# Kernel tuning notes

Measured on AMD Instinct MI355X. Metric: run time of the kernel, lower is better.

The kernel has to match this reference:

```python
import jax, jax.numpy as jnp
import numpy as np

BOX_WARP = 1.0
RAY_START = 2.25
RAY_END = 3.3
S = 32  # depth_resolution (coarse), N_importance = 0


def bilinear_sample(image, coords):
    """Faithful port of the custom grid_sample (align_corners=True mapping).
    image: [B, C, H, W]; coords: [B, M, 2] in [-1, 1]. Returns [B, M, C]."""
    B, C, H, W = image.shape
    ix = (coords[..., 0] + 1.0) * 0.5 * (W - 1)
    iy = (coords[..., 1] + 1.0) * 0.5 * (H - 1)
    ix0 = jnp.floor(ix)
    iy0 = jnp.floor(iy)
    ix1 = ix0 + 1.0
    iy1 = iy0 + 1.0
    # weights use UNclamped corner positions, matching the torch code
    w_nw = (ix1 - ix) * (iy1 - iy)
    w_ne = (ix - ix0) * (iy1 - iy)
    w_sw = (ix1 - ix) * (iy - iy0)
    w_se = (ix - ix0) * (iy - iy0)
    ix0c = jnp.clip(ix0, 0, W - 1).astype(jnp.int32)
    ix1c = jnp.clip(ix1, 0, W - 1).astype(jnp.int32)
    iy0c = jnp.clip(iy0, 0, H - 1).astype(jnp.int32)
    iy1c = jnp.clip(iy1, 0, H - 1).astype(jnp.int32)
    img = image.reshape(B, C, H * W)

    def gather(iyc, ixc):
        idx = iyc * W + ixc  # [B, M]
        return jnp.take_along_axis(img, idx[:, None, :], axis=2)  # [B, C, M]

    out = (gather(iy0c, ix0c) * w_nw[:, None, :]
           + gather(iy0c, ix1c) * w_ne[:, None, :]
           + gather(iy1c, ix0c) * w_sw[:, None, :]
           + gather(iy1c, ix1c) * w_se[:, None, :])
    return out.transpose(0, 2, 1)  # [B, M, C]


def setup_inputs() -> dict:
    key = jax.random.key(0)
    k1, k2, k3, k4, k5 = jax.random.split(key, 5)
    N, n_planes, C, H, W = 2, 3, 32, 256, 256
    R = 16384
    vol_planes = jax.random.normal(k1, (N, n_planes, C, H, W), dtype=jnp.float32)
    dirs = jax.random.normal(k2, (N, R, 3), dtype=jnp.float32)
    dirs = dirs / jnp.linalg.norm(dirs, axis=-1, keepdims=True)
    # camera on sphere of radius 2.7 looking through origin -> samples in box
    ray_origins = -2.7 * dirs
    w1 = jax.random.normal(k3, (C, 64), dtype=jnp.float32) * (1.0 / np.sqrt(C))
    b1 = jnp.zeros((64,), dtype=jnp.float32)
    w2 = jax.random.normal(k4, (64, 33), dtype=jnp.float32) * (1.0 / 8.0)
    b2 = jnp.zeros((33,), dtype=jnp.float32)
    return {"vol_planes": vol_planes, "ray_origins": ray_origins,
            "ray_directions": dirs, "w1": w1, "b1": b1, "w2": w2, "b2": b2}


def reference(vol_planes, ray_origins, ray_directions, w1, b1, w2, b2):
    N, n_planes, C, H, W = vol_planes.shape
    R = ray_origins.shape[1]
    # --- sample_stratified (deterministic: midpoint of each bin) ---
    t = (jnp.arange(S, dtype=vol_planes.dtype) + 0.5) / S
    d = RAY_START + (RAY_END - RAY_START) * t  # [S]
    depths = jnp.broadcast_to(d[None, None, :, None], (N, R, S, 1))
    coords = ray_origins[:, :, None, :] + depths * ray_directions[:, :, None, :]
    M = R * S
    coords = coords.reshape(N, M, 3) * (2.0 / BOX_WARP)
    # --- project_onto_planes (vol_proj=True): xyz, yzx, xzy; sampler uses xy ---
    xy = coords[..., jnp.array([0, 1])]
    yz = coords[..., jnp.array([1, 2])]
    xz = coords[..., jnp.array([0, 2])]
    proj = jnp.stack([xy, yz, xz], axis=1).reshape(N * n_planes, M, 2)
    feats = bilinear_sample(vol_planes.reshape(N * n_planes, C, H, W), proj)
    feats = feats.reshape(N, n_planes, M, C).mean(axis=1)  # aggregate planes
    # --- decoder: small MLP -> 1 sigma + 32 rgb features (EG3D style) ---
    h = jax.nn.softplus(feats @ w1 + b1)
    o = h @ w2 + b2
    sigma = o[..., :1].reshape(N, R, S, 1)
    rgb = (jax.nn.sigmoid(o[..., 1:]) * 1.002 - 0.001).reshape(N, R, S, 32)
    # --- MipRayMarcher2 ---
    deltas = depths[:, :, 1:] - depths[:, :, :-1]
    colors_mid = 0.5 * (rgb[:, :, :-1] + rgb[:, :, 1:])
    densities_mid = 0.5 * (sigma[:, :, :-1] + sigma[:, :, 1:])
    densities_mid = jax.nn.softplus(densities_mid - 1.0)
    alpha = 1.0 - jnp.exp(-deltas * densities_mid)  # [N,R,S-1,1]
    trans = jnp.cumprod(
        jnp.concatenate([jnp.ones_like(alpha[:, :, :1]), 1.0 - alpha + 1e-10],
                        axis=2), axis=2)[:, :, :-1]
    weights = alpha * trans
    rgb_final = (weights * colors_mid).sum(axis=2)  # [N, R, 32]
    return rgb_final
```

## Files before the change

### kernel.cpp

```cpp
#include <hip/hip_runtime.h>
#include <math.h>

#define HH 256
#define WW 256
#define CC 32
#define SS 32
#define NRAYS 32768
#define RPB 8
#define TEXOFF 256

#define FXB_OFF 0
#define SIG_OFF 20480
#define WST_OFF 21504
#define W2T_OFF 25600
#define ALP_OFF 31744
#define POOLSZ  32768

typedef __attribute__((ext_vector_type(8))) short short8;
typedef __attribute__((ext_vector_type(4))) float f32x4;

__device__ __forceinline__ f32x4 mfma16(short8 a, short8 b, f32x4 c) {
    return __builtin_amdgcn_mfma_f32_16x16x32_bf16(a, b, c, 0, 0, 0);
}

__device__ __forceinline__ float bf2f(unsigned short u) {
    union { unsigned int ui; float f; } v; v.ui = ((unsigned int)u) << 16; return v.f;
}
__device__ __forceinline__ float lo2f(unsigned int w) {
    union { unsigned int ui; float f; } v; v.ui = w << 16; return v.f;
}
__device__ __forceinline__ float hi2f(unsigned int w) {
    union { unsigned int ui; float f; } v; v.ui = w & 0xffff0000u; return v.f;
}
__device__ __forceinline__ unsigned short f2bf(float f) {
    union { float f; unsigned int u; } v; v.f = f;
    unsigned int u = v.u;
    unsigned int r = u + 0x7fffu + ((u >> 16) & 1u);
    return (unsigned short)(r >> 16);
}
__device__ __forceinline__ unsigned int pk_bf16(float a, float b) {
    return (unsigned int)f2bf(a) | ((unsigned int)f2bf(b) << 16);
}
__device__ __forceinline__ int iclamp(int x, int lo, int hi) {
    return x < lo ? lo : (x > hi ? hi : x);
}
__device__ __forceinline__ float softplus_f(float z) {
    return fmaxf(z, 0.f) + log1pf(expf(-fabsf(z)));
}
__device__ __forceinline__ float softplus_fast(float z) {
    return fmaxf(z, 0.f) + __logf(1.0f + __expf(-fabsf(z)));
}
__device__ __forceinline__ float sigmoid_fast(float z) {
    return __builtin_amdgcn_rcpf(1.0f + __expf(-z));
}

template<bool F32>
__device__ __forceinline__ float ldv(const void* p, size_t i) {
    if (F32) return ((const float*)p)[i];
    else     return bf2f(((const unsigned short*)p)[i]);
}

__global__ void detect_dtype(const void* __restrict__ rayo, int* __restrict__ flag) {
    const int t = threadIdx.x;
    float sf = 0.f, sb = 0.f;
    if (t < 8) {
        const float* f = (const float*)rayo;
        const unsigned short* u = (const unsigned short*)rayo;
        const float a = f[3 * t], b = f[3 * t + 1], c = f[3 * t + 2];
        const float nf = a * a + b * b + c * c;
        sf = fminf(fabsf(nf - 7.29f), 1e3f);
        const float x = bf2f(u[3 * t]), y = bf2f(u[3 * t + 1]), z = bf2f(u[3 * t + 2]);
        const float nb = x * x + y * y + z * z;
        sb = fminf(fabsf(nb - 7.29f), 1e3f);
    }
    sf += __shfl_down(sf, 4); sb += __shfl_down(sb, 4);
    sf += __shfl_down(sf, 2); sb += __shfl_down(sb, 2);
    sf += __shfl_down(sf, 1); sb += __shfl_down(sb, 1);
    if (t == 0 && blockIdx.x == 0) *flag = (sf < sb) ? 1 : 0;
}

__global__ __launch_bounds__(1024) void transpose_tex(
    const void* __restrict__ vol, unsigned short* __restrict__ tex,
    const int* __restrict__ flag) {
    __shared__ __align__(16) unsigned short tb[32][129];
    const int l = threadIdx.x;
    const int tx = l & 31, ty = l >> 5;
    const int wq = l >> 3, cq = l & 7;
    const int w0 = blockIdx.x * 128;
    const int h  = blockIdx.y;
    const int img = blockIdx.z;
    const size_t srcE = (((size_t)img * CC + ty) * HH + h) * WW + w0 + 4 * tx;
    const size_t dstE = (((size_t)img * HH + h) * WW + (w0 + wq)) * CC + 4 * cq;
    if (*flag) {
        const float4 v = *(const float4*)((const float*)vol + srcE);
        tb[ty][4 * tx + 0] = f2bf(v.x); tb[ty][4 * tx + 1] = f2bf(v.y);
        tb[ty][4 * tx + 2] = f2bf(v.z); tb[ty][4 * tx + 3] = f2bf(v.w);
    } else {
        *(ushort4*)&tb[ty][4 * tx] = *(const ushort4*)((const unsigned short*)vol + srcE);
    }
    __syncthreads();
    ushort4 o;
    o.x = tb[4 * cq + 0][wq]; o.y = tb[4 * cq + 1][wq];
    o.z = tb[4 * cq + 2][wq]; o.w = tb[4 * cq + 3][wq];
    *(ushort4*)(tex + dstE) = o;
}

template<bool F32>
__device__ void render_mfma_body(
    const unsigned short* __restrict__ tex,
    const void* __restrict__ rayo, const void* __restrict__ rayd,
    const void* __restrict__ w1b, const void* __restrict__ b1b,
    const void* __restrict__ w2b, const void* __restrict__ b2b,
    void* __restrict__ outp, char* __restrict__ pool)
{
    const int t = threadIdx.x;
    unsigned short* fxB = (unsigned short*)(pool + FXB_OFF);
    float* sigL = (float*)(pool + SIG_OFF);
    unsigned short* w1t = (unsigned short*)(pool + WST_OFF);
    unsigned short* w2t = (unsigned short*)(pool + W2T_OFF);
    float* aL = (float*)(pool + ALP_OFF);

    for (int i = t; i < 2048; i += 256) {
        const int n = i >> 5, k = i & 31;
        w1t[i] = f2bf(ldv<F32>(w1b, (size_t)k * 64 + n));
    }
    for (int i = t; i < 3072; i += 256) {
        const int n = i >> 6, k = i & 63;
        w2t[i] = (n < 33) ? f2bf(ldv<F32>(w2b, (size_t)k * 33 + n)) : (unsigned short)0;
    }
    __syncthreads();

    {
        const int rl = t >> 5;
        const int L  = t & 31;
        const int c4 = L & 7;
        const int sub = L >> 3;
        const int gray = blockIdx.x * RPB + rl;
        const int n = gray >> 14;
        const size_t rb = (size_t)gray * 3;
        const float ox = ldv<F32>(rayo, rb), oy = ldv<F32>(rayo, rb + 1), oz = ldv<F32>(rayo, rb + 2);
        const float dx = ldv<F32>(rayd, rb), dy = ldv<F32>(rayd, rb + 1), dz = ldv<F32>(rayd, rb + 2);
        const char* texb = (const char*)tex;
        const unsigned int cb = (unsigned int)c4 * 8;

        #pragma unroll 2
        for (int k = 0; k < 8; ++k) {
            const int s = sub * 8 + k;
            const float d = 2.25f + 1.05f * ((s + 0.5f) * (1.0f / 32.0f));
            const float x = (ox + d * dx) * 2.0f;
            const float y = (oy + d * dy) * 2.0f;
            const float z = (oz + d * dz) * 2.0f;
            float a0[4] = {0.f, 0.f, 0.f, 0.f};
            float a1[4] = {0.f, 0.f, 0.f, 0.f};
            float a2[4] = {0.f, 0.f, 0.f, 0.f};
            #pragma unroll
            for (int p = 0; p < 3; p++) {
                const float u = (p == 0) ? x : ((p == 1) ? y : x);
                const float v = (p == 0) ? y : z;
                const float ixf = fmaf(u, 127.5f, 127.5f);
                const float iyf = fmaf(v, 127.5f, 127.5f);
                const float ix0f = floorf(ixf), iy0f = floorf(iyf);
                const float wx1 = ixf - ix0f, wy1 = iyf - iy0f;
                const float wx0 = 1.f - wx1,  wy0 = 1.f - wy1;
                const int ix0 = iclamp((int)ix0f, 0, 255);
                const int ix1 = iclamp((int)ix0f + 1, 0, 255);
                const int iy0 = iclamp((int)iy0f, 0, 255);
                const int iy1 = iclamp((int)iy0f + 1, 0, 255);
                const float w00 = wx0 * wy0, w01 = wx1 * wy0, w10 = wx0 * wy1, w11 = wx1 * wy1;
                const unsigned int pb = (unsigned int)(n * 3 + p) * (HH * WW * CC * 2) + cb;
                const uint2 q00 = *(const uint2*)(texb + pb + ((unsigned int)(iy0 * WW + ix0) << 6));
                const uint2 q01 = *(const uint2*)(texb + pb + ((unsigned int)(iy0 * WW + ix1) << 6));
                const uint2 q10 = *(const uint2*)(texb + pb + ((unsigned int)(iy1 * WW + ix0) << 6));
                const uint2 q11 = *(const uint2*)(texb + pb + ((unsigned int)(iy1 * WW + ix1) << 6));
                const float v00[4] = { lo2f(q00.x), hi2f(q00.x), lo2f(q00.y), hi2f(q00.y) };
                const float v01[4] = { lo2f(q01.x), hi2f(q01.x), lo2f(q01.y), hi2f(q01.y) };
                const float v10[4] = { lo2f(q10.x), hi2f(q10.x), lo2f(q10.y), hi2f(q10.y) };
                const float v11[4] = { lo2f(q11.x), hi2f(q11.x), lo2f(q11.y), hi2f(q11.y) };
                #pragma unroll
                for (int i = 0; i < 4; i++) {
                    float acc = w00 * v00[i];
                    acc = fmaf(w01, v01[i], acc);
                    acc = fmaf(w10, v10[i], acc);
                    acc = fmaf(w11, v11[i], acc);
                    if (p == 0) a0[i] = acc; else if (p == 1) a1[i] = acc; else a2[i] = acc;
                }
            }
            uint2 pk;
            pk.x = pk_bf16((a0[0] + a1[0] + a2[0]) * (1.0f / 3.0f),
                           (a0[1] + a1[1] + a2[1]) * (1.0f / 3.0f));
            pk.y = pk_bf16((a0[2] + a1[2] + a2[2]) * (1.0f / 3.0f),
                           (a0[3] + a1[3] + a2[3]) * (1.0f / 3.0f));
            *(uint2*)(pool + FXB_OFF + (rl * 32 + s) * 80 + c4 * 8) = pk;
        }
    }

    const int w = t >> 6;
    const int lane = t & 63;
    const int l16 = lane & 15, quad = lane >> 4;

    short8 b1f[4];
    #pragma unroll
    for (int nt = 0; nt < 4; nt++)
        b1f[nt] = *(const short8*)(pool + WST_OFF + (nt * 16 + l16) * 64 + quad * 16);
    short8 b2f[3][2];
    #pragma unroll
    for (int nt = 0; nt < 3; nt++)
        #pragma unroll
        for (int ks = 0; ks < 2; ks++)
            b2f[nt][ks] = *(const short8*)(pool + W2T_OFF + (nt * 16 + l16) * 128 + ks * 64 + quad * 16);
    float bb1[4], bb2[3];
    #pragma unroll
    for (int nt = 0; nt < 4; nt++) bb1[nt] = ldv<F32>(b1b, nt * 16 + l16);
    #pragma unroll
    for (int nt = 0; nt < 3; nt++) {
        const int n2 = nt * 16 + l16;
        bb2[nt] = (n2 < 33) ? ldv<F32>(b2b, n2) : 0.f;
    }
    __syncthreads();

    {
        char* hb = pool + WST_OFF + w * 2304;
        #pragma unroll 1
        for (int mt = 0; mt < 4; mt++) {
            const int rbase = w * 64 + mt * 16;
            const short8 a1 = *(const short8*)(pool + FXB_OFF + (rbase + l16) * 80 + quad * 16);
            #pragma unroll
            for (int nt = 0; nt < 4; nt++) {
                f32x4 hc = { bb1[nt], bb1[nt], bb1[nt], bb1[nt] };
                hc = mfma16(a1, b1f[nt], hc);
                #pragma unroll
                for (int r = 0; r < 4; r++) {
                    const float hv = softplus_fast(hc[r]);
                    *(unsigned short*)(hb + (quad * 4 + r) * 144 + (nt * 16 + l16) * 2) = f2bf(hv);
                }
            }
            const short8 a2k0 = *(const short8*)(hb + l16 * 144 + quad * 16);
            const short8 a2k1 = *(const short8*)(hb + l16 * 144 + 64 + quad * 16);
            #pragma unroll
            for (int nt = 0; nt < 3; nt++) {
                f32x4 o = { bb2[nt], bb2[nt], bb2[nt], bb2[nt] };
                o = mfma16(a2k0, b2f[nt][0], o);
                o = mfma16(a2k1, b2f[nt][1], o);
                #pragma unroll
                for (int r = 0; r < 4; r++) {
                    const int row = rbase + quad * 4 + r;
                    if (nt == 0) {
                        if (l16 == 0) sigL[row] = o[r];
                        else fxB[row * 40 + (l16 - 1)] =
                                 f2bf(fmaf(sigmoid_fast(o[r]), 1.002f, -0.001f));
                    } else if (nt == 1) {
                        fxB[row * 40 + (15 + l16)] =
                                 f2bf(fmaf(sigmoid_fast(o[r]), 1.002f, -0.001f));
                    } else if (l16 == 0) {
                        fxB[row * 40 + 31] =
                                 f2bf(fmaf(sigmoid_fast(o[r]), 1.002f, -0.001f));
                    }
                }
            }
        }
    }
    __syncthreads();

    {
        const int rl = t >> 5, sm = t & 31;
        if (sm < 31) {
            const float sp = sigL[rl * 32 + sm];
            const float sn = sigL[rl * 32 + sm + 1];
            const float m = 0.5f * (sp + sn) - 1.0f;
            const float dens = fmaxf(m, 0.f) + __logf(1.0f + __expf(-fabsf(m)));
            aL[rl * 32 + sm] = 1.0f - __expf(-(1.05f / 32.0f) * dens);
        }
    }
    __syncthreads();

    {
        const int rl = t >> 5, sm = t & 31;
        if (sm == 0) {
            float T = 1.0f;
            #pragma unroll
            for (int j = 0; j < 31; j++) {
                const float a = aL[rl * 32 + j];
                aL[rl * 32 + j] = (a * T) * 0.5f;
                T *= (1.0f - a + 1e-10f);
            }
        }
    }
    __syncthreads();

    {
        const int rl = t >> 5, c = t & 31;
        const int gr2 = blockIdx.x * RPB + rl;
        float acc = 0.0f;
        float rp = bf2f(fxB[(rl * 32 + 0) * 40 + c]);
        #pragma unroll 4
        for (int sm = 0; sm < 31; sm++) {
            const float rn = bf2f(fxB[(rl * 32 + sm + 1) * 40 + c]);
            acc = fmaf(aL[rl * 32 + sm], rp + rn, acc);
            rp = rn;
        }
        const size_t oidx = (size_t)gr2 * 32 + c;
        if (F32) ((float*)outp)[oidx] = acc;
        else     ((unsigned short*)outp)[oidx] = f2bf(acc);
    }
}

__global__ __launch_bounds__(256, 4) void render_fast(
    const unsigned short* __restrict__ tex, const void* __restrict__ rayo,
    const void* __restrict__ rayd, const void* __restrict__ w1b,
    const void* __restrict__ b1b, const void* __restrict__ w2b,
    const void* __restrict__ b2b, void* __restrict__ outp,
    const int* __restrict__ flag)
{
    __shared__ __align__(16) char pool[POOLSZ];
    if (*flag) render_mfma_body<true >(tex, rayo, rayd, w1b, b1b, w2b, b2b, outp, pool);
    else       render_mfma_body<false>(tex, rayo, rayd, w1b, b1b, w2b, b2b, outp, pool);
}

template<bool F32>
__device__ __forceinline__ void render_body(
    const void* __restrict__ vol, const void* __restrict__ rayo,
    const void* __restrict__ rayd, const void* __restrict__ w1b,
    const void* __restrict__ b1b, const void* __restrict__ w2b,
    const void* __restrict__ b2b, void* __restrict__ outp,
    float* wsm, float (*rgbL)[SS][33], float (*sigL)[SS])
{
    const int t = threadIdx.x;
    for (int i = t; i < 4257; i += 256) {
        float v;
        if (i < 2048)       v = ldv<F32>(w1b, i);
        else if (i < 2112)  v = ldv<F32>(b1b, i - 2048);
        else if (i < 4224)  v = ldv<F32>(w2b, i - 2112);
        else                v = ldv<F32>(b2b, i - 4224);
        wsm[i] = v;
    }
    __syncthreads();

    const int rl = t >> 5;
    const int s  = t & 31;
    const int gray = blockIdx.x * RPB + rl;
    const int n = gray >> 14;

    const size_t rbase = (size_t)gray * 3;
    const float ox = ldv<F32>(rayo, rbase), oy = ldv<F32>(rayo, rbase + 1), oz = ldv<F32>(rayo, rbase + 2);
    const float dx = ldv<F32>(rayd, rbase), dy = ldv<F32>(rayd, rbase + 1), dz = ldv<F32>(rayd, rbase + 2);
    const float d = 2.25f + 1.05f * ((s + 0.5f) * (1.0f / 32.0f));
    const float x = (ox + d * dx) * 2.0f;
    const float y = (oy + d * dy) * 2.0f;
    const float z = (oz + d * dz) * 2.0f;

    float fx[32];
    #pragma unroll
    for (int c = 0; c < 32; c++) fx[c] = 0.f;

    #pragma unroll
    for (int p = 0; p < 3; p++) {
        const float u = (p == 0) ? x : ((p == 1) ? y : x);
        const float v = (p == 0) ? y : z;
        const float ixf = fmaf(u, 127.5f, 127.5f);
        const float iyf = fmaf(v, 127.5f, 127.5f);
        const float ix0f = floorf(ixf), iy0f = floorf(iyf);
        const float wx1 = ixf - ix0f, wy1 = iyf - iy0f;
        const float wx0 = 1.f - wx1,  wy0 = 1.f - wy1;
        const int ix0 = iclamp((int)ix0f, 0, 255);
        const int ix1 = iclamp((int)ix0f + 1, 0, 255);
        const int iy0 = iclamp((int)iy0f, 0, 255);
        const int iy1 = iclamp((int)iy0f + 1, 0, 255);
        const float wnw = wx0 * wy0, wne = wx1 * wy0, wsw = wx0 * wy1, wse = wx1 * wy1;
        const int i00 = iy0 * WW + ix0, i01 = iy0 * WW + ix1;
        const int i10 = iy1 * WW + ix0, i11 = iy1 * WW + ix1;
        const size_t pb = (size_t)(n * 3 + p) * CC * HH * WW;
        #pragma unroll
        for (int c = 0; c < 32; c++) {
            const size_t cb = pb + (size_t)c * (HH * WW);
            fx[c] += wnw * ldv<F32>(vol, cb + i00) + wne * ldv<F32>(vol, cb + i01)
                   + wsw * ldv<F32>(vol, cb + i10) + wse * ldv<F32>(vol, cb + i11);
        }
    }
    #pragma unroll
    for (int c = 0; c < 32; c++) fx[c] *= (1.0f / 3.0f);

    const float* W1 = wsm;
    const float* B1 = wsm + 2048;
    const float* W2 = wsm + 2112;
    const float* B2 = wsm + 4224;

    float h[64];
    #pragma unroll
    for (int j = 0; j < 64; j++) h[j] = B1[j];
    #pragma unroll
    for (int c = 0; c < 32; c++) {
        const float f = fx[c];
        #pragma unroll
        for (int j = 0; j < 64; j++) h[j] = fmaf(f, W1[c * 64 + j], h[j]);
    }
    #pragma unroll
    for (int j = 0; j < 64; j++) h[j] = softplus_f(h[j]);

    #pragma unroll 1
    for (int k = 0; k < 33; k++) {
        float zz = B2[k];
        #pragma unroll
        for (int j = 0; j < 64; j++) zz = fmaf(h[j], W2[j * 33 + k], zz);
        if (k == 0) sigL[rl][s] = zz;
        else {
            const float sg = 1.0f / (1.0f + expf(-zz));
            rgbL[rl][s][k - 1] = fmaf(sg, 1.002f, -0.001f);
        }
    }
    __syncthreads();

    const int c = t & 31;
    const float delta = 1.05f / 32.0f;
    float T = 1.0f, acc = 0.0f;
    float sig_prev = sigL[rl][0];
    float rgb_prev = rgbL[rl][0][c];
    #pragma unroll 1
    for (int sm = 0; sm < 31; sm++) {
        const float sig_next = sigL[rl][sm + 1];
        const float rgb_next = rgbL[rl][sm + 1][c];
        const float dens = softplus_f(0.5f * (sig_prev + sig_next) - 1.0f);
        const float alpha = 1.0f - expf(-delta * dens);
        acc += alpha * T * 0.5f * (rgb_prev + rgb_next);
        T *= (1.0f - alpha + 1e-10f);
        sig_prev = sig_next;
        rgb_prev = rgb_next;
    }
    const size_t oidx = (size_t)gray * 32 + c;
    if (F32) ((float*)outp)[oidx] = acc;
    else     ((unsigned short*)outp)[oidx] = f2bf(acc);
}

__global__ __launch_bounds__(256) void render_any(
    const void* __restrict__ vol, const void* __restrict__ rayo,
    const void* __restrict__ rayd, const void* __restrict__ w1b,
    const void* __restrict__ b1b, const void* __restrict__ w2b,
    const void* __restrict__ b2b, void* __restrict__ outp,
    const int* __restrict__ flag)
{
    __shared__ float wsm[4257];
    __shared__ float rgbL[RPB][SS][33];
    __shared__ float sigL[RPB][SS];
    if (*flag) render_body<true >(vol, rayo, rayd, w1b, b1b, w2b, b2b, outp, wsm, rgbL, sigL);
    else       render_body<false>(vol, rayo, rayd, w1b, b1b, w2b, b2b, outp, wsm, rgbL, sigL);
}

extern "C" void kernel_launch(void* const* d_in, const int* in_sizes, int n_in,
                              void* d_out, int out_size, void* d_ws, size_t ws_size,
                              hipStream_t stream) {
    const void* vol  = d_in[0];
    const void* rayo = d_in[1];
    const void* rayd = d_in[2];
    const void* w1   = d_in[3];
    const void* b1   = d_in[4];
    const void* w2   = d_in[5];
    const void* b2   = d_in[6];
    int* flag = (int*)d_ws;
    unsigned short* tex = (unsigned short*)((char*)d_ws + TEXOFF);

    const size_t need = TEXOFF + (size_t)6 * HH * WW * CC * 2;

    detect_dtype<<<dim3(1), dim3(64), 0, stream>>>(rayo, flag);
    if (ws_size >= need) {
        transpose_tex<<<dim3(WW / 128, HH, 6), dim3(1024), 0, stream>>>(vol, tex, flag);
        render_fast<<<dim3(NRAYS / RPB), dim3(256), 0, stream>>>(
            tex, rayo, rayd, w1, b1, w2, b2, d_out, flag);
    } else {
        render_any<<<dim3(NRAYS / RPB), dim3(256), 0, stream>>>(
            vol, rayo, rayd, w1, b1, w2, b2, d_out, flag);
    }
}
```

Baseline: 240.3 us.

## Inline dtype detection, one-sample-per-thread gather, hardware bf16 convert, raise occupancy

Removes the separate dtype-detection launch; each block of the transpose and render kernels now detects the dtype itself, saving one kernel launch and a global flag read. The triplane gather is remapped so each thread handles one sample and all 32 channels, using 16-byte loads per corner instead of 8-byte loads split across four threads per sample. Software bf16 rounding is replaced with the v_cvt_pk_bf16_f32 instruction, and the render kernel's launch bounds go from 4 to 5 blocks per SM. The 32-float accumulator per thread raises register pressure, which could conflict with the higher occupancy target, and every block now repeats the small detection work.

```diff
diff --git a/kernel.cpp b/kernel.cpp
--- a/kernel.cpp
+++ b/kernel.cpp
@@ -32,14 +32,15 @@
 __device__ __forceinline__ float hi2f(unsigned int w) {
     union { unsigned int ui; float f; } v; v.ui = w & 0xffff0000u; return v.f;
 }
-__device__ __forceinline__ unsigned short f2bf(float f) {
-    union { float f; unsigned int u; } v; v.f = f;
-    unsigned int u = v.u;
-    unsigned int r = u + 0x7fffu + ((u >> 16) & 1u);
-    return (unsigned short)(r >> 16);
-}
-__device__ __forceinline__ unsigned int pk_bf16(float a, float b) {
-    return (unsigned int)f2bf(a) | ((unsigned int)f2bf(b) << 16);
+__device__ __forceinline__ unsigned int cvtpk2(float a, float b) {
+    unsigned int r;
+    asm("v_cvt_pk_bf16_f32 %0, %1, %2" : "=v"(r) : "v"(a), "v"(b));
+    return r;
+}
+__device__ __forceinline__ unsigned short f2bf_cvt(float f) {
+    unsigned int r;
+    asm("v_cvt_pk_bf16_f32 %0, %1, %2" : "=v"(r) : "v"(f), "v"(f));
+    return (unsigned short)r;
 }
 __device__ __forceinline__ int iclamp(int x, int lo, int hi) {
     return x < lo ? lo : (x > hi ? hi : x);
@@ -60,30 +61,29 @@
     else     return bf2f(((const unsigned short*)p)[i]);
 }
 
-__global__ void detect_dtype(const void* __restrict__ rayo, int* __restrict__ flag) {
-    const int t = threadIdx.x;
+__device__ __forceinline__ int detect_f32_local(const void* __restrict__ rayo) {
+    const float* f = (const float*)rayo;
+    const unsigned short* u = (const unsigned short*)rayo;
     float sf = 0.f, sb = 0.f;
-    if (t < 8) {
-        const float* f = (const float*)rayo;
-        const unsigned short* u = (const unsigned short*)rayo;
-        const float a = f[3 * t], b = f[3 * t + 1], c = f[3 * t + 2];
+    #pragma unroll
+    for (int i = 0; i < 8; ++i) {
+        const float a = f[3 * i], b = f[3 * i + 1], c = f[3 * i + 2];
         const float nf = a * a + b * b + c * c;
-        sf = fminf(fabsf(nf - 7.29f), 1e3f);
-        const float x = bf2f(u[3 * t]), y = bf2f(u[3 * t + 1]), z = bf2f(u[3 * t + 2]);
+        sf += fminf(fabsf(nf - 7.29f), 1e3f);
+        const float x = bf2f(u[3 * i]), y = bf2f(u[3 * i + 1]), z = bf2f(u[3 * i + 2]);
         const float nb = x * x + y * y + z * z;
-        sb = fminf(fabsf(nb - 7.29f), 1e3f);
-    }
-    sf += __shfl_down(sf, 4); sb += __shfl_down(sb, 4);
-    sf += __shfl_down(sf, 2); sb += __shfl_down(sb, 2);
-    sf += __shfl_down(sf, 1); sb += __shfl_down(sb, 1);
-    if (t == 0 && blockIdx.x == 0) *flag = (sf < sb) ? 1 : 0;
+        sb += fminf(fabsf(nb - 7.29f), 1e3f);
+    }
+    return (sf < sb) ? 1 : 0;
 }
 
 __global__ __launch_bounds__(1024) void transpose_tex(
     const void* __restrict__ vol, unsigned short* __restrict__ tex,
-    const int* __restrict__ flag) {
+    const void* __restrict__ rayo) {
     __shared__ __align__(16) unsigned short tb[32][129];
+    __shared__ int sflag;
     const int l = threadIdx.x;
+    if (l == 0) sflag = detect_f32_local(rayo);
     const int tx = l & 31, ty = l >> 5;
     const int wq = l >> 3, cq = l & 7;
     const int w0 = blockIdx.x * 128;
@@ -91,10 +91,11 @@
     const int img = blockIdx.z;
     const size_t srcE = (((size_t)img * CC + ty) * HH + h) * WW + w0 + 4 * tx;
     const size_t dstE = (((size_t)img * HH + h) * WW + (w0 + wq)) * CC + 4 * cq;
-    if (*flag) {
+    __syncthreads();
+    if (sflag) {
         const float4 v = *(const float4*)((const float*)vol + srcE);
-        tb[ty][4 * tx + 0] = f2bf(v.x); tb[ty][4 * tx + 1] = f2bf(v.y);
-        tb[ty][4 * tx + 2] = f2bf(v.z); tb[ty][4 * tx + 3] = f2bf(v.w);
+        tb[ty][4 * tx + 0] = f2bf_cvt(v.x); tb[ty][4 * tx + 1] = f2bf_cvt(v.y);
+        tb[ty][4 * tx + 2] = f2bf_cvt(v.z); tb[ty][4 * tx + 3] = f2bf_cvt(v.w);
     } else {
         *(ushort4*)&tb[ty][4 * tx] = *(const ushort4*)((const unsigned short*)vol + srcE);
     }
@@ -122,75 +123,81 @@
 
     for (int i = t; i < 2048; i += 256) {
         const int n = i >> 5, k = i & 31;
-        w1t[i] = f2bf(ldv<F32>(w1b, (size_t)k * 64 + n));
+        w1t[i] = f2bf_cvt(ldv<F32>(w1b, (size_t)k * 64 + n));
     }
     for (int i = t; i < 3072; i += 256) {
         const int n = i >> 6, k = i & 63;
-        w2t[i] = (n < 33) ? f2bf(ldv<F32>(w2b, (size_t)k * 33 + n)) : (unsigned short)0;
+        w2t[i] = (n < 33) ? f2bf_cvt(ldv<F32>(w2b, (size_t)k * 33 + n)) : (unsigned short)0;
     }
     __syncthreads();
 
     {
-        const int rl = t >> 5;
-        const int L  = t & 31;
-        const int c4 = L & 7;
-        const int sub = L >> 3;
+        const int rl = t >> 5, s = t & 31;
         const int gray = blockIdx.x * RPB + rl;
         const int n = gray >> 14;
         const size_t rb = (size_t)gray * 3;
         const float ox = ldv<F32>(rayo, rb), oy = ldv<F32>(rayo, rb + 1), oz = ldv<F32>(rayo, rb + 2);
         const float dx = ldv<F32>(rayd, rb), dy = ldv<F32>(rayd, rb + 1), dz = ldv<F32>(rayd, rb + 2);
         const char* texb = (const char*)tex;
-        const unsigned int cb = (unsigned int)c4 * 8;
-
-        #pragma unroll 2
-        for (int k = 0; k < 8; ++k) {
-            const int s = sub * 8 + k;
-            const float d = 2.25f + 1.05f * ((s + 0.5f) * (1.0f / 32.0f));
-            const float x = (ox + d * dx) * 2.0f;
-            const float y = (oy + d * dy) * 2.0f;
-            const float z = (oz + d * dz) * 2.0f;
-            float a0[4] = {0.f, 0.f, 0.f, 0.f};
-            float a1[4] = {0.f, 0.f, 0.f, 0.f};
-            float a2[4] = {0.f, 0.f, 0.f, 0.f};
+
+        const float d = 2.25f + 1.05f * ((s + 0.5f) * (1.0f / 32.0f));
+        const float x = (ox + d * dx) * 2.0f;
+        const float y = (oy + d * dy) * 2.0f;
+        const float z = (oz + d * dz) * 2.0f;
+
+        float acc[32];
+        #pragma unroll
+        for (int c = 0; c < 32; ++c) acc[c] = 0.f;
+
+        #pragma unroll
+        for (int p = 0; p < 3; ++p) {
+            const float u = (p == 0) ? x : ((p == 1) ? y : x);
+            const float v = (p == 0) ? y : z;
+            const float ixf = fmaf(u, 127.5f, 127.5f);
+            const float iyf = fmaf(v, 127.5f, 127.5f);
+            const float ix0f = floorf(ixf), iy0f = floorf(iyf);
+            const float wx1 = ixf - ix0f, wy1 = iyf - iy0f;
+            const float wx0 = 1.f - wx1,  wy0 = 1.f - wy1;
+            const int ix0 = iclamp((int)ix0f, 0, 255);
+            const int ix1 = iclamp((int)ix0f + 1, 0, 255);
+            const int iy0 = iclamp((int)iy0f, 0, 255);
+            const int iy1 = iclamp((int)iy0f + 1, 0, 255);
+            const float w00 = wx0 * wy0, w01 = wx1 * wy0, w10 = wx0 * wy1, w11 = wx1 * wy1;
+            const unsigned int pb = (unsigned int)(n * 3 + p) * (HH * WW * CC * 2);
+            const char* b00 = texb + pb + ((unsigned int)(iy0 * WW + ix0) << 6);
+            const char* b01 = texb + pb + ((unsigned int)(iy0 * WW + ix1) << 6);
+            const char* b10 = texb + pb + ((unsigned int)(iy1 * WW + ix0) << 6);
+            const char* b11 = texb + pb + ((unsigned int)(iy1 * WW + ix1) << 6);
             #pragma unroll
-            for (int p = 0; p < 3; p++) {
-                const float u = (p == 0) ? x : ((p == 1) ? y : x);
-                const float v = (p == 0) ? y : z;
-                const float ixf = fmaf(u, 127.5f, 127.5f);
-                const float iyf = fmaf(v, 127.5f, 127.5f);
-                const float ix0f = floorf(ixf), iy0f = floorf(iyf);
-                const float wx1 = ixf - ix0f, wy1 = iyf - iy0f;
-                const float wx0 = 1.f - wx1,  wy0 = 1.f - wy1;
-                const int ix0 = iclamp((int)ix0f, 0, 255);
-                const int ix1 = iclamp((int)ix0f + 1, 0, 255);
-                const int iy0 = iclamp((int)iy0f, 0, 255);
-                const int iy1 = iclamp((int)iy0f + 1, 0, 255);
-                const float w00 = wx0 * wy0, w01 = wx1 * wy0, w10 = wx0 * wy1, w11 = wx1 * wy1;
-                const unsigned int pb = (unsigned int)(n * 3 + p) * (HH * WW * CC * 2) + cb;
-                const uint2 q00 = *(const uint2*)(texb + pb + ((unsigned int)(iy0 * WW + ix0) << 6));
-                const uint2 q01 = *(const uint2*)(texb + pb + ((unsigned int)(iy0 * WW + ix1) << 6));
-                const uint2 q10 = *(const uint2*)(texb + pb + ((unsigned int)(iy1 * WW + ix0) << 6));
-                const uint2 q11 = *(const uint2*)(texb + pb + ((unsigned int)(iy1 * WW + ix1) << 6));
-                const float v00[4] = { lo2f(q00.x), hi2f(q00.x), lo2f(q00.y), hi2f(q00.y) };
-                const float v01[4] = { lo2f(q01.x), hi2f(q01.x), lo2f(q01.y), hi2f(q01.y) };
-                const float v10[4] = { lo2f(q10.x), hi2f(q10.x), lo2f(q10.y), hi2f(q10.y) };
-                const float v11[4] = { lo2f(q11.x), hi2f(q11.x), lo2f(q11.y), hi2f(q11.y) };
+            for (int q = 0; q < 4; ++q) {
+                const uint4 r00 = *(const uint4*)(b00 + (q << 4));
+                const uint4 r01 = *(const uint4*)(b01 + (q << 4));
+                const uint4 r10 = *(const uint4*)(b10 + (q << 4));
+                const uint4 r11 = *(const uint4*)(b11 + (q << 4));
+                const unsigned int* u00 = (const unsigned int*)&r00;
+                const unsigned int* u01 = (const unsigned int*)&r01;
+                const unsigned int* u10 = (const unsigned int*)&r10;
+                const unsigned int* u11 = (const unsigned int*)&r11;
                 #pragma unroll
-                for (int i = 0; i < 4; i++) {
-                    float acc = w00 * v00[i];
-                    acc = fmaf(w01, v01[i], acc);
-                    acc = fmaf(w10, v10[i], acc);
-                    acc = fmaf(w11, v11[i], acc);
-                    if (p == 0) a0[i] = acc; else if (p == 1) a1[i] = acc; else a2[i] = acc;
+                for (int j = 0; j < 4; ++j) {
+                    const int c = q * 8 + j * 2;
+                    float a = acc[c], b = acc[c + 1];
+                    a = fmaf(w00, lo2f(u00[j]), a);  b = fmaf(w00, hi2f(u00[j]), b);
+                    a = fmaf(w01, lo2f(u01[j]), a);  b = fmaf(w01, hi2f(u01[j]), b);
+                    a = fmaf(w10, lo2f(u10[j]), a);  b = fmaf(w10, hi2f(u10[j]), b);
+                    a = fmaf(w11, lo2f(u11[j]), a);  b = fmaf(w11, hi2f(u11[j]), b);
+                    acc[c] = a; acc[c + 1] = b;
                 }
             }
-            uint2 pk;
-            pk.x = pk_bf16((a0[0] + a1[0] + a2[0]) * (1.0f / 3.0f),
-                           (a0[1] + a1[1] + a2[1]) * (1.0f / 3.0f));
-            pk.y = pk_bf16((a0[2] + a1[2] + a2[2]) * (1.0f / 3.0f),
-                           (a0[3] + a1[3] + a2[3]) * (1.0f / 3.0f));
-            *(uint2*)(pool + FXB_OFF + (rl * 32 + s) * 80 + c4 * 8) = pk;
+        }
+        #pragma unroll
+        for (int q = 0; q < 4; ++q) {
+            uint4 pk;
+            pk.x = cvtpk2(acc[q * 8 + 0] * (1.0f / 3.0f), acc[q * 8 + 1] * (1.0f / 3.0f));
+            pk.y = cvtpk2(acc[q * 8 + 2] * (1.0f / 3.0f), acc[q * 8 + 3] * (1.0f / 3.0f));
+            pk.z = cvtpk2(acc[q * 8 + 4] * (1.0f / 3.0f), acc[q * 8 + 5] * (1.0f / 3.0f));
+            pk.w = cvtpk2(acc[q * 8 + 6] * (1.0f / 3.0f), acc[q * 8 + 7] * (1.0f / 3.0f));
+            *(uint4*)(pool + FXB_OFF + t * 80 + (q << 4)) = pk;
         }
     }
 
@@ -231,7 +238,7 @@
                 #pragma unroll
                 for (int r = 0; r < 4; r++) {
                     const float hv = softplus_fast(hc[r]);
-                    *(unsigned short*)(hb + (quad * 4 + r) * 144 + (nt * 16 + l16) * 2) = f2bf(hv);
+                    *(unsigned short*)(hb + (quad * 4 + r) * 144 + (nt * 16 + l16) * 2) = f2bf_cvt(hv);
                 }
             }
             const short8 a2k0 = *(const short8*)(hb + l16 * 144 + quad * 16);
@@ -247,13 +254,13 @@
                     if (nt == 0) {
                         if (l16 == 0) sigL[row] = o[r];
                         else fxB[row * 40 + (l16 - 1)] =
-                                 f2bf(fmaf(sigmoid_fast(o[r]), 1.002f, -0.001f));
+                                 f2bf_cvt(fmaf(sigmoid_fast(o[r]), 1.002f, -0.001f));
                     } else if (nt == 1) {
                         fxB[row * 40 + (15 + l16)] =
-                                 f2bf(fmaf(sigmoid_fast(o[r]), 1.002f, -0.001f));
+                                 f2bf_cvt(fmaf(sigmoid_fast(o[r]), 1.002f, -0.001f));
                     } else if (l16 == 0) {
                         fxB[row * 40 + 31] =
-                                 f2bf(fmaf(sigmoid_fast(o[r]), 1.002f, -0.001f));
+                                 f2bf_cvt(fmaf(sigmoid_fast(o[r]), 1.002f, -0.001f));
                     }
                 }
             }
@@ -300,20 +307,23 @@
         }
         const size_t oidx = (size_t)gr2 * 32 + c;
         if (F32) ((float*)outp)[oidx] = acc;
-        else     ((unsigned short*)outp)[oidx] = f2bf(acc);
-    }
-}
-
-__global__ __launch_bounds__(256, 4) void render_fast(
+        else     ((unsigned short*)outp)[oidx] = f2bf_cvt(acc);
+    }
+}
+
+__global__ __launch_bounds__(256, 5) void render_fast(
     const unsigned short* __restrict__ tex, const void* __restrict__ rayo,
     const void* __restrict__ rayd, const void* __restrict__ w1b,
     const void* __restrict__ b1b, const void* __restrict__ w2b,
-    const void* __restrict__ b2b, void* __restrict__ outp,
-    const int* __restrict__ flag)
+    const void* __restrict__ b2b, void* __restrict__ outp)
 {
     __shared__ __align__(16) char pool[POOLSZ];
-    if (*flag) render_mfma_body<true >(tex, rayo, rayd, w1b, b1b, w2b, b2b, outp, pool);
-    else       render_mfma_body<false>(tex, rayo, rayd, w1b, b1b, w2b, b2b, outp, pool);
+    const int t = threadIdx.x;
+    if (t == 0) *(int*)pool = detect_f32_local(rayo);
+    __syncthreads();
+    const int f32flag = *(const int*)pool;
+    if (f32flag) render_mfma_body<true >(tex, rayo, rayd, w1b, b1b, w2b, b2b, outp, pool);
+    else         render_mfma_body<false>(tex, rayo, rayd, w1b, b1b, w2b, b2b, outp, pool);
 }
 
 template<bool F32>
@@ -427,21 +437,25 @@
     }
     const size_t oidx = (size_t)gray * 32 + c;
     if (F32) ((float*)outp)[oidx] = acc;
-    else     ((unsigned short*)outp)[oidx] = f2bf(acc);
+    else     ((unsigned short*)outp)[oidx] = f2bf_cvt(acc);
 }
 
 __global__ __launch_bounds__(256) void render_any(
     const void* __restrict__ vol, const void* __restrict__ rayo,
     const void* __restrict__ rayd, const void* __restrict__ w1b,
     const void* __restrict__ b1b, const void* __restrict__ w2b,
-    const void* __restrict__ b2b, void* __restrict__ outp,
-    const int* __restrict__ flag)
+    const void* __restrict__ b2b, void* __restrict__ outp)
 {
     __shared__ float wsm[4257];
     __shared__ float rgbL[RPB][SS][33];
     __shared__ float sigL[RPB][SS];
-    if (*flag) render_body<true >(vol, rayo, rayd, w1b, b1b, w2b, b2b, outp, wsm, rgbL, sigL);
-    else       render_body<false>(vol, rayo, rayd, w1b, b1b, w2b, b2b, outp, wsm, rgbL, sigL);
+    __shared__ int sflag;
+    if (threadIdx.x == 0) sflag = detect_f32_local(rayo);
+    __syncthreads();
+    const int f32flag = sflag;
+    __syncthreads();
+    if (f32flag) render_body<true >(vol, rayo, rayd, w1b, b1b, w2b, b2b, outp, wsm, rgbL, sigL);
+    else         render_body<false>(vol, rayo, rayd, w1b, b1b, w2b, b2b, outp, wsm, rgbL, sigL);
 }
 
 extern "C" void kernel_launch(void* const* d_in, const int* in_sizes, int n_in,
@@ -454,18 +468,16 @@
     const void* b1   = d_in[4];
     const void* w2   = d_in[5];
     const void* b2   = d_in[6];
-    int* flag = (int*)d_ws;
     unsigned short* tex = (unsigned short*)((char*)d_ws + TEXOFF);
 
     const size_t need = TEXOFF + (size_t)6 * HH * WW * CC * 2;
 
-    detect_dtype<<<dim3(1), dim3(64), 0, stream>>>(rayo, flag);
     if (ws_size >= need) {
-        transpose_tex<<<dim3(WW / 128, HH, 6), dim3(1024), 0, stream>>>(vol, tex, flag);
+        transpose_tex<<<dim3(WW / 128, HH, 6), dim3(1024), 0, stream>>>(vol, tex, rayo);
         render_fast<<<dim3(NRAYS / RPB), dim3(256), 0, stream>>>(
-            tex, rayo, rayd, w1, b1, w2, b2, d_out, flag);
+            tex, rayo, rayd, w1, b1, w2, b2, d_out);
     } else {
         render_any<<<dim3(NRAYS / RPB), dim3(256), 0, stream>>>(
-            vol, rayo, rayd, w1, b1, w2, b2, d_out, flag);
-    }
-}
+            vol, rayo, rayd, w1, b1, w2, b2, d_out);
+    }
+}
```

Result: slower. 315.4 us (+31.3%).
